# Optimization experiments

Measured on AMD Instinct MI355X. Metric: run time of the kernel, lower is better.

## Reference

```python
import jax, jax.numpy as jnp
import numpy as np

N = 20000      # nodes
E = 320000     # edges
F = 32         # node_feat_dim
H = 128        # hidden_dim
HEADS = 4
DH = 128       # out_channels per head (PyG TransformerConv semantics)
L = 2          # number of GNNBlocks actually built


def _ln(x, s, b, eps=1e-5):
    m = x.mean(-1, keepdims=True)
    v = ((x - m) ** 2).mean(-1, keepdims=True)
    return (x - m) / jnp.sqrt(v + eps) * s + b


def setup_inputs() -> dict:
    key = jax.random.key(0)
    ks = jax.random.split(key, 16)
    nrm = lambda k, sh, sc=0.05: jax.random.normal(k, sh, dtype=jnp.float32) * sc
    inp = {}
    inp['x'] = jax.random.normal(ks[0], (N, F), dtype=jnp.float32)
    inp['edge_index'] = jax.random.randint(ks[1], (2, E), 0, N)
    inp['Win'] = nrm(ks[2], (F, H))
    inp['b_in'] = jnp.zeros((H,), jnp.float32)
    inp['ln1_s'] = jnp.ones((L, H), jnp.float32)
    inp['ln1_b'] = jnp.zeros((L, H), jnp.float32)
    inp['Wq'] = nrm(ks[3], (L, H, HEADS * DH))
    inp['bq'] = jnp.zeros((L, HEADS * DH), jnp.float32)
    inp['Wk'] = nrm(ks[4], (L, H, HEADS * DH))
    inp['bk'] = jnp.zeros((L, HEADS * DH), jnp.float32)
    inp['Wv'] = nrm(ks[5], (L, H, HEADS * DH))
    inp['bv'] = jnp.zeros((L, HEADS * DH), jnp.float32)
    inp['Wskip'] = nrm(ks[6], (L, H, H))
    inp['bskip'] = jnp.zeros((L, H), jnp.float32)
    inp['Wbeta'] = nrm(ks[7], (L, 3 * H, 1))
    inp['ln2_s'] = jnp.ones((L, H), jnp.float32)
    inp['ln2_b'] = jnp.zeros((L, H), jnp.float32)
    inp['W1'] = nrm(ks[8], (L, H, 4 * H))
    inp['b1'] = jnp.zeros((L, 4 * H), jnp.float32)
    inp['W2'] = nrm(ks[9], (L, 4 * H, H))
    inp['b2'] = jnp.zeros((L, H), jnp.float32)
    inp['g1'] = jnp.ones((L,), jnp.float32)
    inp['g2'] = jnp.ones((L,), jnp.float32)
    inp['lno_s'] = jnp.ones((H,), jnp.float32)
    inp['lno_b'] = jnp.zeros((H,), jnp.float32)
    return inp


def reference(x, edge_index, Win, b_in, ln1_s, ln1_b, Wq, bq, Wk, bk, Wv, bv,
              Wskip, bskip, Wbeta, ln2_s, ln2_b, W1, b1, W2, b2, g1, g2,
              lno_s, lno_b):
    src, dst = edge_index[0], edge_index[1]  # messages flow src -> dst
    n = x.shape[0]
    scale = 1.0 / np.sqrt(DH).astype(np.float32)
    h = x @ Win + b_in  # [N,H]
    for l in range(L):
        # --- pre-norm TransformerConv (heads=4, concat=False, beta=True) ---
        hn = _ln(h, ln1_s[l], ln1_b[l])
        q = (hn @ Wq[l] + bq[l]).reshape(n, HEADS, DH)
        k = (hn @ Wk[l] + bk[l]).reshape(n, HEADS, DH)
        v = (hn @ Wv[l] + bv[l]).reshape(n, HEADS, DH)
        # per-edge attention logits [E, HEADS]
        alpha = jnp.einsum('ehd,ehd->eh', q[dst], k[src]) * scale
        # segment softmax over incoming edges of each target node
        amax = jax.ops.segment_max(alpha, dst, num_segments=n)  # [N,HEADS]
        num = jnp.exp(alpha - amax[dst])
        den = jax.ops.segment_sum(num, dst, num_segments=n)      # [N,HEADS]
        a = num / den[dst]                                       # [E,HEADS]
        # scatter-aggregate weighted values, then mean over heads (concat=False)
        agg = jax.ops.segment_sum(a[:, :, None] * v[src], dst, num_segments=n)
        out = agg.mean(axis=1)                                   # [N,H]
        # root skip + beta gate
        xr = hn @ Wskip[l] + bskip[l]
        beta = jax.nn.sigmoid(
            jnp.concatenate([out, xr, out - xr], axis=-1) @ Wbeta[l])  # [N,1]
        attn = beta * xr + (1.0 - beta) * out
        h = h + g1[l] * attn
        # --- pre-norm FFN ---
        hn2 = _ln(h, ln2_s[l], ln2_b[l])
        ffn = jax.nn.gelu(hn2 @ W1[l] + b1[l], approximate=False) @ W2[l] + b2[l]
        h = h + g2[l] * ffn
    return _ln(h, lno_s, lno_b)
```

## Files before the change

### kernel.cpp

```cpp
#include <hip/hip_runtime.h>
#include <hip/hip_bf16.h>
#include <math.h>

#define NN 20000
#define NE 320000

typedef unsigned short ushort_t;
typedef unsigned short ushortx8 __attribute__((ext_vector_type(8)));
typedef short s16x8 __attribute__((ext_vector_type(8)));
typedef float f32x4 __attribute__((ext_vector_type(4)));
typedef float f32x2 __attribute__((ext_vector_type(2)));

__device__ __forceinline__ float us2f(unsigned short u){
  return __uint_as_float(((unsigned)u) << 16);
}
__device__ __forceinline__ unsigned short f2us(float f){
  unsigned u = __float_as_uint(f);
  unsigned r = (u + 0x7fffu + ((u >> 16) & 1u)) >> 16;
  return (unsigned short)r;
}
__device__ __forceinline__ void e4m3x8_to_f32(uint2 d, float* out){
  f32x2 a = __builtin_amdgcn_cvt_pk_f32_fp8(d.x, false);
  f32x2 b = __builtin_amdgcn_cvt_pk_f32_fp8(d.x, true);
  f32x2 c = __builtin_amdgcn_cvt_pk_f32_fp8(d.y, false);
  f32x2 e = __builtin_amdgcn_cvt_pk_f32_fp8(d.y, true);
  out[0] = a.x; out[1] = a.y; out[2] = b.x; out[3] = b.y;
  out[4] = c.x; out[5] = c.y; out[6] = e.x; out[7] = e.y;
}
__device__ __forceinline__ uint2 f32x8_to_e4m3(const float* f){
  unsigned lo = __builtin_amdgcn_cvt_pk_fp8_f32(f[0], f[1], 0u, false);
  lo = __builtin_amdgcn_cvt_pk_fp8_f32(f[2], f[3], lo, true);
  unsigned hi = __builtin_amdgcn_cvt_pk_fp8_f32(f[4], f[5], 0u, false);
  hi = __builtin_amdgcn_cvt_pk_fp8_f32(f[6], f[7], hi, true);
  return make_uint2(lo, hi);
}

__global__ void k_hist(const int* __restrict__ ei, int* __restrict__ deg){
  int e = blockIdx.x * 256 + threadIdx.x;
  if (e < NE) atomicAdd(&deg[ei[NE + e]], 1);
}

__global__ __launch_bounds__(1024) void k_scan(const int* __restrict__ deg,
                                               int* __restrict__ rowst,
                                               int* __restrict__ cur){
  __shared__ int s[1024];
  __shared__ int carry_s;
  int tid = threadIdx.x;
  if (tid == 0) carry_s = 0;
  __syncthreads();
  for (int base = 0; base < NN; base += 1024){
    int v = (base + tid < NN) ? deg[base + tid] : 0;
    s[tid] = v; __syncthreads();
    for (int off = 1; off < 1024; off <<= 1){
      int t = (tid >= off) ? s[tid - off] : 0;
      __syncthreads();
      s[tid] += t;
      __syncthreads();
    }
    int carry = carry_s;
    int excl = carry + s[tid] - v;
    if (base + tid < NN){ rowst[base + tid] = excl; cur[base + tid] = excl; }
    __syncthreads();
    if (tid == 0) carry_s = carry + s[1023];
    __syncthreads();
  }
  if (tid == 0) rowst[NN] = carry_s;
}

__global__ void k_scatter(const int* __restrict__ ei, int* __restrict__ cur,
                          int* __restrict__ srcs){
  int e = blockIdx.x * 256 + threadIdx.x;
  if (e < NE){
    int s = ei[e];
    int d = ei[NE + e];
    int p = atomicAdd(&cur[d], 1);
    srcs[p] = s;
  }
}

__global__ void k_wt(const float* __restrict__ Wq, const float* __restrict__ Wk,
                     const float* __restrict__ Wv, const float* __restrict__ Wsk,
                     const float* __restrict__ W1, const float* __restrict__ W2,
                     const float* __restrict__ bq, const float* __restrict__ bk,
                     const float* __restrict__ bv, const float* __restrict__ bsk,
                     ushort_t* __restrict__ out, float* __restrict__ bcat,
                     int* __restrict__ deg){
  int f = blockIdx.x * 256 + threadIdx.x;
  if (f < 688128){
    float val;
    if (f < 425984){
      int l = f / 212992, idx = f % 212992;
      int n = idx / 128, kk = idx % 128;
      if (n < 512)       val = Wq[(size_t)l * 65536 + kk * 512 + n];
      else if (n < 1024) val = Wk[(size_t)l * 65536 + kk * 512 + (n - 512)];
      else if (n < 1536) val = Wv[(size_t)l * 65536 + kk * 512 + (n - 1024)];
      else               val = Wsk[(size_t)l * 16384 + kk * 128 + (n - 1536)];
    } else if (f < 557056){
      int idx = f - 425984;
      int l = idx / 65536, r = idx % 65536;
      int n = r / 128, kk = r % 128;
      val = W1[(size_t)l * 65536 + kk * 512 + n];
    } else {
      int idx = f - 557056;
      int l = idx / 65536, r = idx % 65536;
      int n = r / 512, kk = r % 512;
      val = W2[(size_t)l * 65536 + kk * 128 + n];
    }
    out[f] = f2us(val);
  } else if (f < 691456){
    int i = f - 688128;
    int l = i / 1664, c = i % 1664;
    float v;
    if (c < 512)       v = bq[l * 512 + c];
    else if (c < 1024) v = bk[l * 512 + c - 512];
    else if (c < 1536) v = bv[l * 512 + c - 1024];
    else               v = bsk[l * 128 + c - 1536];
    bcat[i] = v;
  } else if (f < 711456){
    deg[f - 691456] = 0;
  }
}

__global__ __launch_bounds__(128) void k_inproj(const float* __restrict__ x,
                                                const float* __restrict__ Win,
                                                const float* __restrict__ bin,
                                                float* __restrict__ h){
  __shared__ float sW[32 * 128];
  __shared__ float sx[4][32];
  int tid = threadIdx.x;
  for (int i = 0; i < 32; i++) sW[i * 128 + tid] = Win[i * 128 + tid];
  int r0 = blockIdx.x * 4;
  {
    int r = tid >> 5, kk = tid & 31;
    int gr = r0 + r;
    sx[r][kk] = (gr < NN) ? x[gr * 32 + kk] : 0.f;
  }
  __syncthreads();
  float bias = bin[tid];
  for (int r = 0; r < 4; r++){
    int gr = r0 + r;
    if (gr >= NN) break;
    float acc = bias;
    #pragma unroll
    for (int k2 = 0; k2 < 32; k2++) acc += sx[r][k2] * sW[k2 * 128 + tid];
    h[(size_t)gr * 128 + tid] = acc;
  }
}

__global__ void k_ln(const float* __restrict__ in, const float* __restrict__ sc,
                     const float* __restrict__ bi, ushort_t* __restrict__ outp, int rows){
  int row = blockIdx.x * 4 + (threadIdx.x >> 6);
  int lane = threadIdx.x & 63;
  if (row >= rows) return;
  const float* p = in + (size_t)row * 128 + lane * 2;
  float x0 = p[0], x1 = p[1];
  float sum = x0 + x1;
  for (int m = 1; m < 64; m <<= 1) sum += __shfl_xor(sum, m);
  float mean = sum * (1.f / 128.f);
  float d0 = x0 - mean, d1 = x1 - mean;
  float vs = d0 * d0 + d1 * d1;
  for (int m = 1; m < 64; m <<= 1) vs += __shfl_xor(vs, m);
  float rstd = rsqrtf(vs * (1.f / 128.f) + 1e-5f);
  int d = lane * 2;
  ushort_t* o = outp + (size_t)row * 128 + d;
  o[0] = f2us(d0 * rstd * sc[d] + bi[d]);
  o[1] = f2us(d1 * rstd * sc[d + 1] + bi[d + 1]);
}

template<int MODE, int LNOUT>
__global__ __launch_bounds__(256) void k_mm(const ushort_t* __restrict__ A, int M, int K,
                                            const ushort_t* __restrict__ Bt,
                                            const float* __restrict__ bias,
                                            void* __restrict__ Cp, int ldc,
                                            const float* __restrict__ gptr,
                                            ushort_t* __restrict__ qout,
                                            unsigned char* __restrict__ kvout,
                                            ushort_t* __restrict__ xrout,
                                            const float* __restrict__ lnsc,
                                            const float* __restrict__ lnbi,
                                            void* __restrict__ lnout){
  constexpr int SMEM = (MODE == 4) ? (128 * 132 * 4) : (2 * 128 * 72 * 2);
  __shared__ __align__(16) char smem_raw[SMEM];
  ushort_t* As = (ushort_t*)smem_raw;
  ushort_t* Bs = As + 128 * 72;
  int tid = threadIdx.x;
  int m0 = blockIdx.x * 128, n0 = blockIdx.y * 128;
  int lane = tid & 63, w = tid >> 6;
  int wm = (w >> 1) * 64, wn = (w & 1) * 64;
  int fr = lane & 15, fq = lane >> 4;
  f32x4 acc[4][4];
  #pragma unroll
  for (int i = 0; i < 4; i++)
    #pragma unroll
    for (int j = 0; j < 4; j++) acc[i][j] = (f32x4){0.f, 0.f, 0.f, 0.f};

  for (int k0 = 0; k0 < K; k0 += 64){
    __syncthreads();
    #pragma unroll
    for (int it = 0; it < 4; it++){
      int idx = it * 256 + tid;
      int row = idx >> 3, ks = (idx & 7) * 8;
      int gr = m0 + row; if (gr >= M) gr = M - 1;
      *(ushortx8*)&As[row * 72 + ks] = *(const ushortx8*)(A + (size_t)gr * K + k0 + ks);
      *(ushortx8*)&Bs[row * 72 + ks] = *(const ushortx8*)(Bt + (size_t)(n0 + row) * K + k0 + ks);
    }
    __syncthreads();
    #pragma unroll
    for (int ks = 0; ks < 64; ks += 32){
      s16x8 a[4], b[4];
      #pragma unroll
      for (int i = 0; i < 4; i++)
        a[i] = *(const s16x8*)&As[(wm + i * 16 + fr) * 72 + ks + fq * 8];
      #pragma unroll
      for (int j = 0; j < 4; j++)
        b[j] = *(const s16x8*)&Bs[(wn + j * 16 + fr) * 72 + ks + fq * 8];
      #pragma unroll
      for (int i = 0; i < 4; i++)
        #pragma unroll
        for (int j = 0; j < 4; j++)
          acc[i][j] = __builtin_amdgcn_mfma_f32_16x16x32_bf16(a[i], b[j], acc[i][j], 0, 0, 0);
    }
  }

  if (MODE == 4){
    float g = *gptr;
    float* fhs = (float*)smem_raw;
    __syncthreads();
    #pragma unroll
    for (int i = 0; i < 4; i++){
      #pragma unroll
      for (int r = 0; r < 4; r++){
        int lrow = wm + i * 16 + fq * 4 + r;
        int gr = m0 + lrow;
        if (gr >= M) continue;
        #pragma unroll
        for (int j = 0; j < 4; j++){
          int gc = wn + j * 16 + fr;
          float c = acc[i][j][r] + bias[gc];
          float hv = ((float*)Cp)[(size_t)gr * 128 + gc] + g * c;
          ((float*)Cp)[(size_t)gr * 128 + gc] = hv;
          fhs[lrow * 132 + gc] = hv;
        }
      }
    }
    __syncthreads();
    for (int rr = 0; rr < 32; rr++){
      int lrow = w * 32 + rr;
      int gr = m0 + lrow;
      if (gr >= M) break;
      int d = lane * 2;
      float x0 = fhs[lrow * 132 + d], x1 = fhs[lrow * 132 + d + 1];
      float sum = x0 + x1;
      for (int msk = 1; msk < 64; msk <<= 1) sum += __shfl_xor(sum, msk);
      float mean = sum * (1.f / 128.f);
      float d0 = x0 - mean, d1 = x1 - mean;
      float vs = d0 * d0 + d1 * d1;
      for (int msk = 1; msk < 64; msk <<= 1) vs += __shfl_xor(vs, msk);
      float rstd = rsqrtf(vs * (1.f / 128.f) + 1e-5f);
      float o0 = d0 * rstd * lnsc[d] + lnbi[d];
      float o1 = d1 * rstd * lnsc[d + 1] + lnbi[d + 1];
      if (LNOUT){
        ushort_t* o = (ushort_t*)lnout + (size_t)gr * 128 + d;
        o[0] = f2us(o0); o[1] = f2us(o1);
      } else {
        float* o = (float*)lnout + (size_t)gr * 128 + d;
        o[0] = o0; o[1] = o1;
      }
    }
    return;
  }

  __syncthreads();
  ushort_t* Cs = (ushort_t*)smem_raw;
  #pragma unroll
  for (int i = 0; i < 4; i++){
    int rowb = wm + i * 16 + fq * 4;
    #pragma unroll
    for (int j = 0; j < 4; j++){
      int col = wn + j * 16 + fr;
      float bv = bias[n0 + col];
      #pragma unroll
      for (int r = 0; r < 4; r++){
        float c = acc[i][j][r] + bv;
        if (MODE == 1) c = 0.5f * c * (1.f + erff(c * 0.70710678118654752f));
        Cs[(rowb + r) * 136 + col] = f2us(c);
      }
    }
  }
  __syncthreads();
  #pragma unroll
  for (int it = 0; it < 8; it++){
    int idx = it * 256 + tid;
    int row = idx >> 4, seg = idx & 15;
    int gr = m0 + row;
    if (gr >= M) continue;
    ushortx8 cv = *(const ushortx8*)&Cs[row * 136 + seg * 8];
    int gc = n0 + seg * 8;
    if (MODE == 1){
      *(ushortx8*)((ushort_t*)Cp + (size_t)gr * ldc + gc) = cv;
    } else {
      if (n0 < 512){
        *(ushortx8*)(qout + (size_t)gr * 512 + gc) = cv;
      } else if (n0 < 1536){
        float fv[8];
        #pragma unroll
        for (int t = 0; t < 8; t++) fv[t] = us2f(cv[t]);
        *(uint2*)(kvout + (size_t)gr * 1024 + (gc - 512)) = f32x8_to_e4m3(fv);
      } else {
        *(ushortx8*)(xrout + (size_t)gr * 128 + (gc - 1536)) = cv;
      }
    }
  }
}

__global__ void k_attn(const ushort_t* __restrict__ q, const unsigned char* __restrict__ kv8,
                       const int* __restrict__ rowst, const int* __restrict__ srcs,
                       const ushort_t* __restrict__ xr, const float* __restrict__ Wb,
                       const float* __restrict__ g1p, float* __restrict__ h,
                       const float* __restrict__ sc2, const float* __restrict__ bi2,
                       ushort_t* __restrict__ hn){
  int n = blockIdx.x * 4 + (threadIdx.x >> 6);
  int lane = threadIdx.x & 63;
  if (n >= NN) return;
  int s0 = rowst[n], s1 = rowst[n + 1];
  int deg = s1 - s0;
  int head = lane >> 4;
  const float scale = 0.08838834764831845f;
  ushortx8 qv = *((const ushortx8*)(q + (size_t)n * 512) + lane);
  float qf[8];
  #pragma unroll
  for (int t = 0; t < 8; t++) qf[t] = us2f(qv[t]);
  float l = 0.f;
  float acc[8] = {0.f, 0.f, 0.f, 0.f, 0.f, 0.f, 0.f, 0.f};
  for (int c0 = s0; c0 < s1; c0 += 64){
    int rem = s1 - c0; if (rem > 64) rem = 64;
    int se = (lane < rem) ? srcs[c0 + lane] : 0;
    int j = 0;
    for (; j + 4 <= rem; j += 4){
      int sv[4];
      #pragma unroll
      for (int u = 0; u < 4; u++) sv[u] = __shfl(se, j + u);
      uint2 kd[4], vd[4];
      #pragma unroll
      for (int u = 0; u < 4; u++){
        const unsigned char* base = kv8 + (size_t)sv[u] * 1024;
        kd[u] = *((const uint2*)(base) + lane);
        vd[u] = *((const uint2*)(base + 512) + lane);
      }
      float p[4];
      #pragma unroll
      for (int u = 0; u < 4; u++){
        float kf[8];
        e4m3x8_to_f32(kd[u], kf);
        float s = 0.f;
        #pragma unroll
        for (int t = 0; t < 8; t++) s += qf[t] * kf[t];
        p[u] = s;
      }
      #pragma unroll
      for (int u = 0; u < 4; u++){
        p[u] += __shfl_xor(p[u], 1); p[u] += __shfl_xor(p[u], 2);
        p[u] += __shfl_xor(p[u], 4); p[u] += __shfl_xor(p[u], 8);
      }
      #pragma unroll
      for (int u = 0; u < 4; u++){
        float vf[8];
        e4m3x8_to_f32(vd[u], vf);
        float ww = __expf(p[u] * scale);
        l += ww;
        #pragma unroll
        for (int t = 0; t < 8; t++) acc[t] += ww * vf[t];
      }
    }
    for (; j < rem; j++){
      int sv0 = __shfl(se, j);
      const unsigned char* base = kv8 + (size_t)sv0 * 1024;
      uint2 kd = *((const uint2*)(base) + lane);
      uint2 vd = *((const uint2*)(base + 512) + lane);
      float kf[8];
      e4m3x8_to_f32(kd, kf);
      float p0 = 0.f;
      #pragma unroll
      for (int t = 0; t < 8; t++) p0 += qf[t] * kf[t];
      p0 += __shfl_xor(p0, 1); p0 += __shfl_xor(p0, 2);
      p0 += __shfl_xor(p0, 4); p0 += __shfl_xor(p0, 8);
      float vf[8];
      e4m3x8_to_f32(vd, vf);
      float ww = __expf(p0 * scale);
      l += ww;
      #pragma unroll
      for (int t = 0; t < 8; t++) acc[t] += ww * vf[t];
    }
  }
  float inv = deg ? (0.25f / l) : 0.f;
  #pragma unroll
  for (int t = 0; t < 8; t++){
    float r = acc[t] * inv;
    r += __shfl_xor(r, 16); r += __shfl_xor(r, 32);
    acc[t] = r;
  }
  if (lane < 16){
    int d = lane * 8;
    float xv[8];
    {
      ushortx8 xrv = *(const ushortx8*)(xr + (size_t)n * 128 + d);
      #pragma unroll
      for (int t = 0; t < 8; t++) xv[t] = us2f(xrv[t]);
    }
    float pp = 0.f;
    #pragma unroll
    for (int t = 0; t < 8; t++){
      float w0 = Wb[d + t], w1 = Wb[128 + d + t], w2 = Wb[256 + d + t];
      pp += acc[t] * (w0 + w2) + xv[t] * (w1 - w2);
    }
    pp += __shfl_xor(pp, 1); pp += __shfl_xor(pp, 2);
    pp += __shfl_xor(pp, 4); pp += __shfl_xor(pp, 8);
    float beta = 1.f / (1.f + __expf(-pp));
    float g = *g1p;
    float* hp = h + (size_t)n * 128 + d;
    float hv[8];
    {
      float4 h0 = *(const float4*)(hp);
      float4 h1 = *(const float4*)(hp + 4);
      hv[0]=h0.x; hv[1]=h0.y; hv[2]=h0.z; hv[3]=h0.w;
      hv[4]=h1.x; hv[5]=h1.y; hv[6]=h1.z; hv[7]=h1.w;
    }
    #pragma unroll
    for (int t = 0; t < 8; t++)
      hv[t] += g * (beta * xv[t] + (1.f - beta) * acc[t]);
    float s = 0.f;
    #pragma unroll
    for (int t = 0; t < 8; t++) s += hv[t];
    s += __shfl_xor(s, 1); s += __shfl_xor(s, 2);
    s += __shfl_xor(s, 4); s += __shfl_xor(s, 8);
    float mean = s * (1.f / 128.f);
    float vs = 0.f;
    #pragma unroll
    for (int t = 0; t < 8; t++){ float dd = hv[t] - mean; vs += dd * dd; }
    vs += __shfl_xor(vs, 1); vs += __shfl_xor(vs, 2);
    vs += __shfl_xor(vs, 4); vs += __shfl_xor(vs, 8);
    float rstd = rsqrtf(vs * (1.f / 128.f) + 1e-5f);
    *(float4*)(hp) = make_float4(hv[0], hv[1], hv[2], hv[3]);
    *(float4*)(hp + 4) = make_float4(hv[4], hv[5], hv[6], hv[7]);
    ushortx8 hno;
    #pragma unroll
    for (int t = 0; t < 8; t++)
      hno[t] = f2us((hv[t] - mean) * rstd * sc2[d + t] + bi2[d + t]);
    *(ushortx8*)(hn + (size_t)n * 128 + d) = hno;
  }
}

extern "C" void kernel_launch(void* const* d_in, const int* in_sizes, int n_in,
                              void* d_out, int out_size, void* d_ws, size_t ws_size,
                              hipStream_t stream){
  const float* x    = (const float*)d_in[0];
  const int*   ei   = (const int*)d_in[1];
  const float* Win  = (const float*)d_in[2];
  const float* bin  = (const float*)d_in[3];
  const float* ln1s = (const float*)d_in[4];
  const float* ln1b = (const float*)d_in[5];
  const float* Wq   = (const float*)d_in[6];
  const float* bq   = (const float*)d_in[7];
  const float* Wk   = (const float*)d_in[8];
  const float* bk   = (const float*)d_in[9];
  const float* Wv   = (const float*)d_in[10];
  const float* bv   = (const float*)d_in[11];
  const float* Wsk  = (const float*)d_in[12];
  const float* bsk  = (const float*)d_in[13];
  const float* Wbt  = (const float*)d_in[14];
  const float* ln2s = (const float*)d_in[15];
  const float* ln2b = (const float*)d_in[16];
  const float* W1   = (const float*)d_in[17];
  const float* b1   = (const float*)d_in[18];
  const float* W2   = (const float*)d_in[19];
  const float* b2   = (const float*)d_in[20];
  const float* g1   = (const float*)d_in[21];
  const float* g2   = (const float*)d_in[22];
  const float* lnos = (const float*)d_in[23];
  const float* lnob = (const float*)d_in[24];

  char* wsb = (char*)d_ws;
  size_t off = 0;
  float*         h    = (float*)(wsb + off);         off += (size_t)NN * 128 * 4;
  ushort_t*      hn   = (ushort_t*)(wsb + off);      off += (size_t)NN * 128 * 2;
  ushort_t*      qbuf = (ushort_t*)(wsb + off);      off += (size_t)NN * 512 * 2;
  unsigned char* kv8  = (unsigned char*)(wsb + off); off += (size_t)NN * 1024;
  ushort_t*      xrb  = (ushort_t*)(wsb + off);      off += (size_t)NN * 128 * 2;
  ushort_t*      tb   = (ushort_t*)(wsb + off);      off += (size_t)NN * 512 * 2;
  ushort_t*      wt   = (ushort_t*)(wsb + off);      off += (size_t)688128 * 2;
  float*         bcat = (float*)(wsb + off);         off += (size_t)3328 * 4;
  int*           deg   = (int*)(wsb + off);          off += (size_t)NN * 4;
  int*           rowst = (int*)(wsb + off);          off += (size_t)(NN + 4) * 4;
  int*           cur   = (int*)(wsb + off);          off += (size_t)NN * 4;
  int*           srcs  = (int*)(wsb + off);          off += (size_t)NE * 4;
  ushort_t* Wcat = wt;
  ushort_t* W1t  = wt + 425984;
  ushort_t* W2t  = wt + 557056;

  k_wt<<<2780, 256, 0, stream>>>(Wq, Wk, Wv, Wsk, W1, W2, bq, bk, bv, bsk, wt, bcat, deg);
  k_hist<<<(NE + 255) / 256, 256, 0, stream>>>(ei, deg);
  k_scan<<<1, 1024, 0, stream>>>(deg, rowst, cur);
  k_scatter<<<(NE + 255) / 256, 256, 0, stream>>>(ei, cur, srcs);
  k_inproj<<<(NN + 3) / 4, 128, 0, stream>>>(x, Win, bin, h);
  k_ln<<<(NN + 3) / 4, 256, 0, stream>>>(h, ln1s, ln1b, hn, NN);

  dim3 gQ(157, 13), gF1(157, 4), gF2(157, 1);
  for (int l = 0; l < 2; l++){
    k_mm<3,0><<<gQ, 256, 0, stream>>>(hn, NN, 128, Wcat + (size_t)l * 212992, bcat + l * 1664,
                                      nullptr, 0, nullptr, qbuf, kv8, xrb,
                                      nullptr, nullptr, nullptr);
    k_attn<<<(NN + 3) / 4, 256, 0, stream>>>(qbuf, kv8, rowst, srcs, xrb, Wbt + l * 384,
                                             g1 + l, h, ln2s + l * 128, ln2b + l * 128, hn);
    k_mm<1,0><<<gF1, 256, 0, stream>>>(hn, NN, 128, W1t + (size_t)l * 65536, b1 + l * 512,
                                       tb, 512, nullptr, nullptr, nullptr, nullptr,
                                       nullptr, nullptr, nullptr);
    if (l == 0){
      k_mm<4,1><<<gF2, 256, 0, stream>>>(tb, NN, 512, W2t, b2, h, 128, g2,
                                         nullptr, nullptr, nullptr,
                                         ln1s + 128, ln1b + 128, hn);
    } else {
      k_mm<4,0><<<gF2, 256, 0, stream>>>(tb, NN, 512, W2t + 65536, b2 + 128, h, 128, g2 + 1,
                                         nullptr, nullptr, nullptr,
                                         lnos, lnob, d_out);
    }
  }
}
```

Baseline: 471.5 us.

## Split fused edge attention into separate logit and aggregation kernels

Splits the single per-node attention kernel into two passes. The first computes exponentiated attention weights per edge and head from q and fp8 K and stores them in a new float buffer. The second gathers only the V rows and reuses the stored weights. Both passes now unroll over 8 edges instead of 4, aiming to cut per-kernel register pressure and raise memory-level parallelism. In exchange it adds one kernel launch and a write plus re-read of the edge weight buffer (NE*4 floats), while the srcs list is read twice.

```diff
diff --git a/kernel.cpp b/kernel.cpp
--- a/kernel.cpp
+++ b/kernel.cpp
@@ -313,7 +313,68 @@
   }
 }
 
-__global__ void k_attn(const ushort_t* __restrict__ q, const unsigned char* __restrict__ kv8,
+__global__ void k_alpha(const ushort_t* __restrict__ q, const unsigned char* __restrict__ kv8,
+                        const int* __restrict__ rowst, const int* __restrict__ srcs,
+                        float* __restrict__ alw){
+  int n = blockIdx.x * 4 + (threadIdx.x >> 6);
+  int lane = threadIdx.x & 63;
+  if (n >= NN) return;
+  int s0 = rowst[n], s1 = rowst[n + 1];
+  if (s0 == s1) return;
+  ushortx8 qv = *((const ushortx8*)(q + (size_t)n * 512) + lane);
+  float qf[8];
+  #pragma unroll
+  for (int t = 0; t < 8; t++) qf[t] = us2f(qv[t]);
+  const float scale = 0.08838834764831845f;
+  int head = lane >> 4;
+  for (int c0 = s0; c0 < s1; c0 += 64){
+    int rem = s1 - c0; if (rem > 64) rem = 64;
+    int se = (lane < rem) ? srcs[c0 + lane] : 0;
+    int j = 0;
+    for (; j + 8 <= rem; j += 8){
+      int sv[8];
+      #pragma unroll
+      for (int u = 0; u < 8; u++) sv[u] = __shfl(se, j + u);
+      uint2 kd[8];
+      #pragma unroll
+      for (int u = 0; u < 8; u++)
+        kd[u] = *((const uint2*)(kv8 + (size_t)sv[u] * 1024) + lane);
+      float p[8];
+      #pragma unroll
+      for (int u = 0; u < 8; u++){
+        float kf[8];
+        e4m3x8_to_f32(kd[u], kf);
+        float s = 0.f;
+        #pragma unroll
+        for (int t = 0; t < 8; t++) s += qf[t] * kf[t];
+        p[u] = s;
+      }
+      #pragma unroll
+      for (int u = 0; u < 8; u++){
+        p[u] += __shfl_xor(p[u], 1); p[u] += __shfl_xor(p[u], 2);
+        p[u] += __shfl_xor(p[u], 4); p[u] += __shfl_xor(p[u], 8);
+      }
+      if ((lane & 15) == 0){
+        #pragma unroll
+        for (int u = 0; u < 8; u++) alw[(size_t)(c0 + j + u) * 4 + head] = __expf(p[u] * scale);
+      }
+    }
+    for (; j < rem; j++){
+      int sv0 = __shfl(se, j);
+      uint2 kd = *((const uint2*)(kv8 + (size_t)sv0 * 1024) + lane);
+      float kf[8];
+      e4m3x8_to_f32(kd, kf);
+      float p0 = 0.f;
+      #pragma unroll
+      for (int t = 0; t < 8; t++) p0 += qf[t] * kf[t];
+      p0 += __shfl_xor(p0, 1); p0 += __shfl_xor(p0, 2);
+      p0 += __shfl_xor(p0, 4); p0 += __shfl_xor(p0, 8);
+      if ((lane & 15) == 0) alw[(size_t)(c0 + j) * 4 + head] = __expf(p0 * scale);
+    }
+  }
+}
+
+__global__ void k_node(const float* __restrict__ alw, const unsigned char* __restrict__ kv8,
                        const int* __restrict__ rowst, const int* __restrict__ srcs,
                        const ushort_t* __restrict__ xr, const float* __restrict__ Wb,
                        const float* __restrict__ g1p, float* __restrict__ h,
@@ -325,68 +386,38 @@
   int s0 = rowst[n], s1 = rowst[n + 1];
   int deg = s1 - s0;
   int head = lane >> 4;
-  const float scale = 0.08838834764831845f;
-  ushortx8 qv = *((const ushortx8*)(q + (size_t)n * 512) + lane);
-  float qf[8];
-  #pragma unroll
-  for (int t = 0; t < 8; t++) qf[t] = us2f(qv[t]);
   float l = 0.f;
   float acc[8] = {0.f, 0.f, 0.f, 0.f, 0.f, 0.f, 0.f, 0.f};
   for (int c0 = s0; c0 < s1; c0 += 64){
     int rem = s1 - c0; if (rem > 64) rem = 64;
     int se = (lane < rem) ? srcs[c0 + lane] : 0;
     int j = 0;
-    for (; j + 4 <= rem; j += 4){
-      int sv[4];
-      #pragma unroll
-      for (int u = 0; u < 4; u++) sv[u] = __shfl(se, j + u);
-      uint2 kd[4], vd[4];
-      #pragma unroll
-      for (int u = 0; u < 4; u++){
-        const unsigned char* base = kv8 + (size_t)sv[u] * 1024;
-        kd[u] = *((const uint2*)(base) + lane);
-        vd[u] = *((const uint2*)(base + 512) + lane);
-      }
-      float p[4];
-      #pragma unroll
-      for (int u = 0; u < 4; u++){
-        float kf[8];
-        e4m3x8_to_f32(kd[u], kf);
-        float s = 0.f;
-        #pragma unroll
-        for (int t = 0; t < 8; t++) s += qf[t] * kf[t];
-        p[u] = s;
-      }
-      #pragma unroll
-      for (int u = 0; u < 4; u++){
-        p[u] += __shfl_xor(p[u], 1); p[u] += __shfl_xor(p[u], 2);
-        p[u] += __shfl_xor(p[u], 4); p[u] += __shfl_xor(p[u], 8);
-      }
-      #pragma unroll
-      for (int u = 0; u < 4; u++){
+    for (; j + 8 <= rem; j += 8){
+      int sv[8];
+      #pragma unroll
+      for (int u = 0; u < 8; u++) sv[u] = __shfl(se, j + u);
+      uint2 vd[8];
+      #pragma unroll
+      for (int u = 0; u < 8; u++)
+        vd[u] = *((const uint2*)(kv8 + (size_t)sv[u] * 1024 + 512) + lane);
+      float wv[8];
+      #pragma unroll
+      for (int u = 0; u < 8; u++) wv[u] = alw[(size_t)(c0 + j + u) * 4 + head];
+      #pragma unroll
+      for (int u = 0; u < 8; u++){
         float vf[8];
         e4m3x8_to_f32(vd[u], vf);
-        float ww = __expf(p[u] * scale);
-        l += ww;
+        l += wv[u];
         #pragma unroll
-        for (int t = 0; t < 8; t++) acc[t] += ww * vf[t];
+        for (int t = 0; t < 8; t++) acc[t] += wv[u] * vf[t];
       }
     }
     for (; j < rem; j++){
       int sv0 = __shfl(se, j);
-      const unsigned char* base = kv8 + (size_t)sv0 * 1024;
-      uint2 kd = *((const uint2*)(base) + lane);
-      uint2 vd = *((const uint2*)(base + 512) + lane);
-      float kf[8];
-      e4m3x8_to_f32(kd, kf);
-      float p0 = 0.f;
-      #pragma unroll
-      for (int t = 0; t < 8; t++) p0 += qf[t] * kf[t];
-      p0 += __shfl_xor(p0, 1); p0 += __shfl_xor(p0, 2);
-      p0 += __shfl_xor(p0, 4); p0 += __shfl_xor(p0, 8);
+      uint2 vd = *((const uint2*)(kv8 + (size_t)sv0 * 1024 + 512) + lane);
       float vf[8];
       e4m3x8_to_f32(vd, vf);
-      float ww = __expf(p0 * scale);
+      float ww = alw[(size_t)(c0 + j) * 4 + head];
       l += ww;
       #pragma unroll
       for (int t = 0; t < 8; t++) acc[t] += ww * vf[t];
@@ -487,6 +518,7 @@
   unsigned char* kv8  = (unsigned char*)(wsb + off); off += (size_t)NN * 1024;
   ushort_t*      xrb  = (ushort_t*)(wsb + off);      off += (size_t)NN * 128 * 2;
   ushort_t*      tb   = (ushort_t*)(wsb + off);      off += (size_t)NN * 512 * 2;
+  float*         alw  = (float*)(wsb + off);         off += (size_t)NE * 4 * 4;
   ushort_t*      wt   = (ushort_t*)(wsb + off);      off += (size_t)688128 * 2;
   float*         bcat = (float*)(wsb + off);         off += (size_t)3328 * 4;
   int*           deg   = (int*)(wsb + off);          off += (size_t)NN * 4;
@@ -509,7 +541,8 @@
     k_mm<3,0><<<gQ, 256, 0, stream>>>(hn, NN, 128, Wcat + (size_t)l * 212992, bcat + l * 1664,
                                       nullptr, 0, nullptr, qbuf, kv8, xrb,
                                       nullptr, nullptr, nullptr);
-    k_attn<<<(NN + 3) / 4, 256, 0, stream>>>(qbuf, kv8, rowst, srcs, xrb, Wbt + l * 384,
+    k_alpha<<<(NN + 3) / 4, 256, 0, stream>>>(qbuf, kv8, rowst, srcs, alw);
+    k_node<<<(NN + 3) / 4, 256, 0, stream>>>(alw, kv8, rowst, srcs, xrb, Wbt + l * 384,
                                              g1 + l, h, ln2s + l * 128, ln2b + l * 128, hn);
     k_mm<1,0><<<gF1, 256, 0, stream>>>(hn, NN, 128, W1t + (size_t)l * 65536, b1 + l * 512,
                                        tb, 512, nullptr, nullptr, nullptr, nullptr,
```

Measured after the change: 487.7 us. 1.03x slower.
